# Performance work log

Measured on AMD Instinct MI355X. Metric: run time of the kernel, lower is better.

## Reference

```python
import jax, jax.numpy as jnp
import numpy as np

EPS = 1e-12  # torch F.normalize eps


def setup_inputs() -> dict:
    key = jax.random.key(0)
    k1, k2, k3 = jax.random.split(key, 3)
    B, way, shot, D, H, W = 64, 5, 1, 640, 5, 5
    nq = 75
    base = jax.random.normal(k1, (B, way, shot, D, H, W), dtype=jnp.float32)
    query = jax.random.normal(k2, (B, nq, D, H, W), dtype=jnp.float32)
    r = jax.random.normal(k3, (2,), dtype=jnp.float32) * 0.1
    return {"base": base, "query": query, "r": r, "neighbor_k": 5}


def reference(base, query, r, neighbor_k):
    B, way, shot, D, H, W = base.shape
    nq = query.shape[1]
    hw = H * W

    # ---- global-cosine branch: spatial-mean descriptors ----
    base_mean = base.reshape(B, way * shot, D, hw).mean(axis=-1)   # [B, way*shot, D]
    query_mean = query.reshape(B, nq, D, hw).mean(axis=-1)         # [B, nq, D]
    bm = base_mean / jnp.maximum(jnp.linalg.norm(base_mean, axis=-1, keepdims=True), EPS)
    qm = query_mean / jnp.maximum(jnp.linalg.norm(query_mean, axis=-1, keepdims=True), EPS)
    logits = jnp.einsum('bqd,bkd->bqk', qm, bm)                    # [B, nq, way*shot]

    # ---- DN4 image-to-class branch (vectorized over the original triple loop) ----
    # query local descriptors: [B, nq, hw, D], L2-normalized over channels
    q = query.reshape(B, nq, D, hw).transpose(0, 1, 3, 2)
    q = q / jnp.linalg.norm(q, axis=-1, keepdims=True)
    # support local descriptors: base_mix [B, way, shot*D, hw], column-normalized
    s = base.reshape(B, way, shot * D, hw)
    s = s / jnp.linalg.norm(s, axis=2, keepdims=True)
    # cosine sims between every query patch and every support patch of each class
    # (requires shot*D == D, i.e. shot == 1, as in the original code)
    sim = jnp.einsum('bqpd,bkdl->bqkpl', q, s)                     # [B, nq, way, hw, hw]
    topk_vals, _ = jax.lax.top_k(sim, neighbor_k)                  # [B, nq, way, hw, k]
    logits_dn4 = topk_vals.sum(axis=(-1, -2)) / neighbor_k         # [B, nq, way]

    return r[0] * logits + r[1] * logits_dn4
```

## Files before the change

kernel.cpp:

```cpp
#include <hip/hip_runtime.h>
#include <hip/hip_bf16.h>
#include <math.h>

#define NB    64
#define WAY   5
#define DCH   640
#define HW    25
#define NQ    75
#define NBK   5
#define EPSN  1e-12f

#define QPB   4
#define BPB   ((NQ + QPB - 1) / QPB)
#define NWK   (NB * BPB)
#define NDG   (DCH / 8)
#define SCOLS 128
#define CD    64
#define NCHK  (DCH / CD)
#define CFL   (CD * HW)

typedef __attribute__((ext_vector_type(8)))  short  bf16x8;
typedef __attribute__((ext_vector_type(8)))  ushort u16x8;
typedef __attribute__((ext_vector_type(16))) float  f32x16;
typedef __attribute__((ext_vector_type(4)))  float  f32x4;

#define AS1 __attribute__((address_space(1)))
#define AS3 __attribute__((address_space(3)))

__device__ inline ushort f2bf(float f) {
    uint u = __float_as_uint(f);
    return (ushort)((u + 0x7FFFu + ((u >> 16) & 1u)) >> 16);
}

__global__ __launch_bounds__(256) void k_prep(const float* __restrict__ base,
                                              float* __restrict__ invs,
                                              float* __restrict__ invsm,
                                              ushort* __restrict__ sT)
{
    const int bk = blockIdx.x;
    const int b  = bk / WAY;
    const int k  = bk - b * WAY;
    const float* src = base + (size_t)bk * (DCH * HW);
    __shared__ float lds[DCH * HW];
    __shared__ float red[256];
    const int tid = threadIdx.x;

    const f32x4* s4 = (const f32x4*)src;
    f32x4* l4 = (f32x4*)lds;
    for (int i = tid; i < (DCH * HW) / 4; i += 256)
        l4[i] = __builtin_nontemporal_load(s4 + i);
    __syncthreads();

    if (tid < HW) {
        float ss = 0.f;
        for (int d = 0; d < DCH; ++d) { float v = lds[d * HW + tid]; ss = fmaf(v, v, ss); }
        invs[bk * HW + tid] = rsqrtf(ss);
    }

    float ssq = 0.f;
    for (int d = tid; d < DCH; d += 256) {
        float s = 0.f;
        #pragma unroll
        for (int pp = 0; pp < HW; ++pp) s += lds[d * HW + pp];
        float m = s * (1.0f / HW);
        ssq = fmaf(m, m, ssq);
    }
    red[tid] = ssq;
    __syncthreads();
    for (int s = 128; s > 0; s >>= 1) {
        if (tid < s) red[tid] += red[tid + s];
        __syncthreads();
    }
    if (tid == 0) invsm[bk] = 1.0f / fmaxf(sqrtf(red[0]), EPSN);

    ushort* dstb = sT + (size_t)b * (NDG * SCOLS * 8);
    for (int t = tid; t < NDG * HW; t += 256) {
        const int dg = t / HW, l = t - dg * HW;
        u16x8 v;
        #pragma unroll
        for (int e = 0; e < 8; ++e) v[e] = f2bf(lds[(dg * 8 + e) * HW + l]);
        *(u16x8*)&dstb[((size_t)dg * SCOLS + k * HW + l) * 8] = v;
    }
    if (k == 0) {
        const u16x8 z = (u16x8)(ushort)0;
        for (int t = tid; t < NDG * 3; t += 256) {
            const int dg = t / 3, sc = 125 + (t - dg * 3);
            *(u16x8*)&dstb[((size_t)dg * SCOLS + sc) * 8] = z;
        }
    }
}

__global__ __launch_bounds__(256, 2) void k_fused(const float* __restrict__ query,
                                                  const ushort* __restrict__ sT,
                                                  const float* __restrict__ invs,
                                                  const float* __restrict__ invsm,
                                                  const float* __restrict__ r,
                                                  float* __restrict__ out)
{
    __shared__ __align__(16) float lds_q[QPB][2][CFL];
    __shared__ float invs_l[SCOLS];
    __shared__ float invsm_l[WAY];

    const int tid  = threadIdx.x;
    const int wid  = tid >> 6;
    const int lane = tid & 63;
    const int p    = lane & 31;
    const int hi   = lane >> 5;

    const int wk = (blockIdx.x & 7) * (int)(gridDim.x >> 3) + (blockIdx.x >> 3);
    const int b  = wk / BPB;
    const int qb = wk - b * BPB;
    const int q  = qb * QPB + wid;
    const bool qok = q < NQ;

    if (tid < WAY * HW) invs_l[tid] = invs[b * WAY * HW + tid];
    if (tid >= WAY * HW && tid < SCOLS) invs_l[tid] = 0.f;
    if (tid < WAY)      invsm_l[tid] = invsm[b * WAY + tid];
    __syncthreads();
    if (!qok) return;

    f32x16 acc0 = {}, acc1 = {}, acc2 = {}, acc3 = {}, accg = {};

    const int pc = (p < HW) ? p : (HW - 1);
    const float* qrow = query + (size_t)(b * NQ + q) * (DCH * HW);
    const ushort* sTb = sT + (size_t)b * (NDG * SCOLS * 8);

#define ISSUE(c)                                                               \
    {                                                                          \
        const float* src_ = qrow + (c) * CFL;                                  \
        float* dst_ = &lds_q[wid][(c) & 1][0];                                 \
        _Pragma("unroll")                                                      \
        for (int i = 0; i < 6; ++i)                                            \
            __builtin_amdgcn_global_load_lds(                                  \
                (const AS1 uint*)(src_ + i * 256 + lane * 4),                  \
                (AS3 uint*)(dst_ + i * 256), 16, 0, 0);                        \
        if (lane < 16)                                                         \
            __builtin_amdgcn_global_load_lds(                                  \
                (const AS1 uint*)(src_ + 1536 + lane * 4),                     \
                (AS3 uint*)(dst_ + 1536), 16, 0, 0);                           \
    }

    ISSUE(0)

    for (int c = 0; c < NCHK; ++c) {
        bf16x8 af[16];
        #pragma unroll
        for (int ks = 0; ks < CD / 16; ++ks) {
            const int dg = c * 8 + ks * 2 + hi;
            const bf16x8* arow = (const bf16x8*)(sTb + (size_t)dg * SCOLS * 8);
            af[ks * 4 + 0] = arow[p];
            af[ks * 4 + 1] = arow[32 + p];
            af[ks * 4 + 2] = arow[64 + p];
            af[ks * 4 + 3] = arow[96 + p];
        }

        if (c + 1 < NCHK) {
            asm volatile("s_waitcnt lgkmcnt(0)" ::: "memory");
            ISSUE(c + 1)
            asm volatile("s_waitcnt vmcnt(7)" ::: "memory");
        } else {
            asm volatile("s_waitcnt vmcnt(0)" ::: "memory");
        }
        __builtin_amdgcn_sched_barrier(0);

        const float* qb_lds = &lds_q[wid][c & 1][hi * 8 * HW + pc];
        #pragma unroll
        for (int ks = 0; ks < CD / 16; ++ks) {
            const float v0 = qb_lds[(ks * 16 + 0) * HW];
            const float v1 = qb_lds[(ks * 16 + 1) * HW];
            const float v2 = qb_lds[(ks * 16 + 2) * HW];
            const float v3 = qb_lds[(ks * 16 + 3) * HW];
            const float v4 = qb_lds[(ks * 16 + 4) * HW];
            const float v5 = qb_lds[(ks * 16 + 5) * HW];
            const float v6 = qb_lds[(ks * 16 + 6) * HW];
            const float v7 = qb_lds[(ks * 16 + 7) * HW];
            union { uint u[4]; bf16x8 v; } bqu;
            asm("v_cvt_pk_bf16_f32 %0, %1, %2" : "=v"(bqu.u[0]) : "v"(v0), "v"(v1));
            asm("v_cvt_pk_bf16_f32 %0, %1, %2" : "=v"(bqu.u[1]) : "v"(v2), "v"(v3));
            asm("v_cvt_pk_bf16_f32 %0, %1, %2" : "=v"(bqu.u[2]) : "v"(v4), "v"(v5));
            asm("v_cvt_pk_bf16_f32 %0, %1, %2" : "=v"(bqu.u[3]) : "v"(v6), "v"(v7));
            const bf16x8 bq = bqu.v;
            acc0 = __builtin_amdgcn_mfma_f32_32x32x16_bf16(af[ks * 4 + 0], bq, acc0, 0, 0, 0);
            acc1 = __builtin_amdgcn_mfma_f32_32x32x16_bf16(af[ks * 4 + 1], bq, acc1, 0, 0, 0);
            acc2 = __builtin_amdgcn_mfma_f32_32x32x16_bf16(af[ks * 4 + 2], bq, acc2, 0, 0, 0);
            acc3 = __builtin_amdgcn_mfma_f32_32x32x16_bf16(af[ks * 4 + 3], bq, acc3, 0, 0, 0);
            accg = __builtin_amdgcn_mfma_f32_32x32x16_bf16(bq, bq, accg, 0, 0, 0);
        }
    }
#undef ISSUE

    const bool pok = p < HW;

    float diag = 0.f, qq = 0.f;
    #pragma unroll
    for (int rr = 0; rr < 16; ++rr) {
        const int rowb = (rr & 3) + 8 * (rr >> 2);
        const int row  = rowb + 4 * hi;
        diag = (row == p) ? accg[rr] : diag;
        if (row < HW && pok) qq += accg[rr];
    }
    diag += __shfl_xor(diag, 32);
    const float invq = rsqrtf(diag);

    float gs[WAY] = {0.f, 0.f, 0.f, 0.f, 0.f};
#define TILE_SUM(ACC, T)                                            \
    _Pragma("unroll")                                               \
    for (int rr = 0; rr < 16; ++rr) {                               \
        const int s0 = (T) * 32 + (rr & 3) + 8 * (rr >> 2);         \
        const float v0 = (hi || !pok) ? 0.f : ACC[rr];              \
        const float v1 = (hi && pok) ? ACC[rr] : 0.f;               \
        if (s0 < 125)     gs[s0 / 25]       += v0;                  \
        if (s0 + 4 < 125) gs[(s0 + 4) / 25] += v1;                  \
    }
    TILE_SUM(acc0, 0) TILE_SUM(acc1, 1) TILE_SUM(acc2, 2) TILE_SUM(acc3, 3)
#undef TILE_SUM

    #pragma unroll
    for (int o = 1; o < 64; o <<= 1) {
        qq += __shfl_xor(qq, o);
        #pragma unroll
        for (int g = 0; g < WAY; ++g) gs[g] += __shfl_xor(gs[g], o);
    }

#define SCALE(ACC, T)                                               \
    _Pragma("unroll")                                               \
    for (int rr = 0; rr < 16; ++rr) {                               \
        const int s0 = (T) * 32 + (rr & 3) + 8 * (rr >> 2);         \
        ACC[rr] *= invs_l[s0 + 4 * hi];                             \
    }
    SCALE(acc0, 0) SCALE(acc1, 1) SCALE(acc2, 2) SCALE(acc3, 3)
#undef SCALE

    float tots[WAY];
    #pragma unroll
    for (int g = 0; g < WAY; ++g) {
        float t0 = -3.402823466e38f, t1 = t0, t2 = t0, t3 = t0, t4 = t0;
        #pragma unroll
        for (int j = 0; j < HW; ++j) {
            const int scol = g * HW + j;
            const int t = scol >> 5, row = scol & 31;
            const int hreq = (row >> 2) & 1;
            const int rr = (row & 3) | ((row >> 3) << 2);
            const float av = (t == 0) ? acc0[rr] : (t == 1) ? acc1[rr]
                           : (t == 2) ? acc2[rr] : acc3[rr];
            float mine = (hi == hreq) ? av : 0.f;
            mine += __shfl_xor(mine, 32);
            float x = mine, a;
            a = fmaxf(t0, x); x = fminf(t0, x); t0 = a;
            a = fmaxf(t1, x); x = fminf(t1, x); t1 = a;
            a = fmaxf(t2, x); x = fminf(t2, x); t2 = a;
            a = fmaxf(t3, x); x = fminf(t3, x); t3 = a;
            a = fmaxf(t4, x); x = fminf(t4, x); t4 = a;
        }
        tots[g] = pok ? (t0 + t1 + t2 + t3 + t4) * invq : 0.f;
    }
    #pragma unroll
    for (int o = 1; o < 64; o <<= 1) {
        #pragma unroll
        for (int g = 0; g < WAY; ++g) tots[g] += __shfl_xor(tots[g], o);
    }

    const float r0 = r[0], r1 = r[1];
    const float invqm = 1.0f / fmaxf(sqrtf(qq) * (1.0f / HW), EPSN);
    float res[WAY];
    #pragma unroll
    for (int g = 0; g < WAY; ++g)
        res[g] = r0 * gs[g] * (1.0f / 625.0f) * invqm * invsm_l[g]
               + r1 * tots[g] * 0.5f * (1.0f / NBK);

    float ov = res[0];
    ov = (lane == 1) ? res[1] : ov;
    ov = (lane == 2) ? res[2] : ov;
    ov = (lane == 3) ? res[3] : ov;
    ov = (lane == 4) ? res[4] : ov;
    if (lane < WAY) out[(size_t)(b * NQ + q) * WAY + lane] = ov;
}

extern "C" void kernel_launch(void* const* d_in, const int* in_sizes, int n_in,
                              void* d_out, int out_size, void* d_ws, size_t ws_size,
                              hipStream_t stream)
{
    const float* base  = (const float*)d_in[0];
    const float* query = (const float*)d_in[1];
    const float* r     = (const float*)d_in[2];
    float* out = (float*)d_out;

    float* invs   = (float*)d_ws;
    float* invsm  = invs + NB * WAY * HW;
    ushort* sT    = (ushort*)((float*)d_ws + 16384);

    k_prep<<<NB * WAY, 256, 0, stream>>>(base, invs, invsm, sT);
    k_fused<<<NWK, 256, 0, stream>>>(query, sT, invs, invsm, r, out);
}
```

Before: 112.0 us.

## Double-buffer support fragments in registers and halve query chunk size

Halves the channel chunk staged in LDS and prefetches the next chunk's bf16 support fragments into a second register bank while the current chunk's MFMAs run. The loop is manually unrolled by two to alternate banks, the vmcnt wait is adjusted to cover both queued loads, and setprio raises wave priority during the MFMA block. This aims to hide global-load latency of the support fragments, which was previously exposed at the start of each chunk. It adds more loop iterations and waits, and it can raise register pressure.

```diff
diff --git a/kernel.cpp b/kernel.cpp
--- a/kernel.cpp
+++ b/kernel.cpp
@@ -15,7 +15,7 @@
 #define NWK   (NB * BPB)
 #define NDG   (DCH / 8)
 #define SCOLS 128
-#define CD    64
+#define CD    32
 #define NCHK  (DCH / CD)
 #define CFL   (CD * HW)
 
@@ -130,64 +130,85 @@
         const float* src_ = qrow + (c) * CFL;                                  \
         float* dst_ = &lds_q[wid][(c) & 1][0];                                 \
         _Pragma("unroll")                                                      \
-        for (int i = 0; i < 6; ++i)                                            \
+        for (int i = 0; i < 3; ++i)                                            \
             __builtin_amdgcn_global_load_lds(                                  \
                 (const AS1 uint*)(src_ + i * 256 + lane * 4),                  \
                 (AS3 uint*)(dst_ + i * 256), 16, 0, 0);                        \
-        if (lane < 16)                                                         \
+        if (lane < 8)                                                          \
             __builtin_amdgcn_global_load_lds(                                  \
-                (const AS1 uint*)(src_ + 1536 + lane * 4),                     \
-                (AS3 uint*)(dst_ + 1536), 16, 0, 0);                           \
-    }
-
+                (const AS1 uint*)(src_ + 768 + lane * 4),                      \
+                (AS3 uint*)(dst_ + 768), 16, 0, 0);                            \
+    }
+
+#define LOAD_AF(BANK, c)                                                       \
+    {                                                                          \
+        _Pragma("unroll")                                                      \
+        for (int ks = 0; ks < 2; ++ks) {                                       \
+            const int dg = (c) * 4 + ks * 2 + hi;                              \
+            const bf16x8* arow = (const bf16x8*)(sTb + (size_t)dg * SCOLS * 8);\
+            BANK[ks * 4 + 0] = arow[p];                                        \
+            BANK[ks * 4 + 1] = arow[32 + p];                                   \
+            BANK[ks * 4 + 2] = arow[64 + p];                                   \
+            BANK[ks * 4 + 3] = arow[96 + p];                                   \
+        }                                                                      \
+    }
+
+#define COMPUTE(c, BANK)                                                       \
+    {                                                                          \
+        __builtin_amdgcn_s_setprio(1);                                         \
+        const float* qb_lds = &lds_q[wid][(c) & 1][hi * 8 * HW + pc];          \
+        _Pragma("unroll")                                                      \
+        for (int ks = 0; ks < 2; ++ks) {                                       \
+            const float v0 = qb_lds[(ks * 16 + 0) * HW];                       \
+            const float v1 = qb_lds[(ks * 16 + 1) * HW];                       \
+            const float v2 = qb_lds[(ks * 16 + 2) * HW];                       \
+            const float v3 = qb_lds[(ks * 16 + 3) * HW];                       \
+            const float v4 = qb_lds[(ks * 16 + 4) * HW];                       \
+            const float v5 = qb_lds[(ks * 16 + 5) * HW];                       \
+            const float v6 = qb_lds[(ks * 16 + 6) * HW];                       \
+            const float v7 = qb_lds[(ks * 16 + 7) * HW];                       \
+            union { uint u[4]; bf16x8 v; } bqu;                                \
+            asm("v_cvt_pk_bf16_f32 %0, %1, %2" : "=v"(bqu.u[0]) : "v"(v0), "v"(v1)); \
+            asm("v_cvt_pk_bf16_f32 %0, %1, %2" : "=v"(bqu.u[1]) : "v"(v2), "v"(v3)); \
+            asm("v_cvt_pk_bf16_f32 %0, %1, %2" : "=v"(bqu.u[2]) : "v"(v4), "v"(v5)); \
+            asm("v_cvt_pk_bf16_f32 %0, %1, %2" : "=v"(bqu.u[3]) : "v"(v6), "v"(v7)); \
+            const bf16x8 bq = bqu.v;                                           \
+            acc0 = __builtin_amdgcn_mfma_f32_32x32x16_bf16(BANK[ks * 4 + 0], bq, acc0, 0, 0, 0); \
+            acc1 = __builtin_amdgcn_mfma_f32_32x32x16_bf16(BANK[ks * 4 + 1], bq, acc1, 0, 0, 0); \
+            acc2 = __builtin_amdgcn_mfma_f32_32x32x16_bf16(BANK[ks * 4 + 2], bq, acc2, 0, 0, 0); \
+            acc3 = __builtin_amdgcn_mfma_f32_32x32x16_bf16(BANK[ks * 4 + 3], bq, acc3, 0, 0, 0); \
+            accg = __builtin_amdgcn_mfma_f32_32x32x16_bf16(bq, bq, accg, 0, 0, 0); \
+        }                                                                      \
+        __builtin_amdgcn_s_setprio(0);                                         \
+    }
+
+#define STEP(c, CUR, NXT)                                                      \
+    {                                                                          \
+        if ((c) + 1 < NCHK) {                                                  \
+            asm volatile("s_waitcnt lgkmcnt(0)" ::: "memory");                 \
+            ISSUE((c) + 1)                                                     \
+            LOAD_AF(NXT, (c) + 1)                                              \
+            asm volatile("s_waitcnt vmcnt(12)" ::: "memory");                  \
+        } else {                                                               \
+            asm volatile("s_waitcnt vmcnt(0)" ::: "memory");                   \
+        }                                                                      \
+        __builtin_amdgcn_sched_barrier(0);                                     \
+        COMPUTE(c, CUR)                                                        \
+    }
+
+    bf16x8 afA[8], afB[8];
     ISSUE(0)
-
-    for (int c = 0; c < NCHK; ++c) {
-        bf16x8 af[16];
-        #pragma unroll
-        for (int ks = 0; ks < CD / 16; ++ks) {
-            const int dg = c * 8 + ks * 2 + hi;
-            const bf16x8* arow = (const bf16x8*)(sTb + (size_t)dg * SCOLS * 8);
-            af[ks * 4 + 0] = arow[p];
-            af[ks * 4 + 1] = arow[32 + p];
-            af[ks * 4 + 2] = arow[64 + p];
-            af[ks * 4 + 3] = arow[96 + p];
-        }
-
-        if (c + 1 < NCHK) {
-            asm volatile("s_waitcnt lgkmcnt(0)" ::: "memory");
-            ISSUE(c + 1)
-            asm volatile("s_waitcnt vmcnt(7)" ::: "memory");
-        } else {
-            asm volatile("s_waitcnt vmcnt(0)" ::: "memory");
-        }
-        __builtin_amdgcn_sched_barrier(0);
-
-        const float* qb_lds = &lds_q[wid][c & 1][hi * 8 * HW + pc];
-        #pragma unroll
-        for (int ks = 0; ks < CD / 16; ++ks) {
-            const float v0 = qb_lds[(ks * 16 + 0) * HW];
-            const float v1 = qb_lds[(ks * 16 + 1) * HW];
-            const float v2 = qb_lds[(ks * 16 + 2) * HW];
-            const float v3 = qb_lds[(ks * 16 + 3) * HW];
-            const float v4 = qb_lds[(ks * 16 + 4) * HW];
-            const float v5 = qb_lds[(ks * 16 + 5) * HW];
-            const float v6 = qb_lds[(ks * 16 + 6) * HW];
-            const float v7 = qb_lds[(ks * 16 + 7) * HW];
-            union { uint u[4]; bf16x8 v; } bqu;
-            asm("v_cvt_pk_bf16_f32 %0, %1, %2" : "=v"(bqu.u[0]) : "v"(v0), "v"(v1));
-            asm("v_cvt_pk_bf16_f32 %0, %1, %2" : "=v"(bqu.u[1]) : "v"(v2), "v"(v3));
-            asm("v_cvt_pk_bf16_f32 %0, %1, %2" : "=v"(bqu.u[2]) : "v"(v4), "v"(v5));
-            asm("v_cvt_pk_bf16_f32 %0, %1, %2" : "=v"(bqu.u[3]) : "v"(v6), "v"(v7));
-            const bf16x8 bq = bqu.v;
-            acc0 = __builtin_amdgcn_mfma_f32_32x32x16_bf16(af[ks * 4 + 0], bq, acc0, 0, 0, 0);
-            acc1 = __builtin_amdgcn_mfma_f32_32x32x16_bf16(af[ks * 4 + 1], bq, acc1, 0, 0, 0);
-            acc2 = __builtin_amdgcn_mfma_f32_32x32x16_bf16(af[ks * 4 + 2], bq, acc2, 0, 0, 0);
-            acc3 = __builtin_amdgcn_mfma_f32_32x32x16_bf16(af[ks * 4 + 3], bq, acc3, 0, 0, 0);
-            accg = __builtin_amdgcn_mfma_f32_32x32x16_bf16(bq, bq, accg, 0, 0, 0);
-        }
+    LOAD_AF(afA, 0)
+
+    #pragma unroll 1
+    for (int c = 0; c < NCHK; c += 2) {
+        STEP(c,     afA, afB)
+        STEP(c + 1, afB, afA)
     }
 #undef ISSUE
+#undef LOAD_AF
+#undef COMPUTE
+#undef STEP
 
     const bool pok = p < HW;
 
```

After: 108.0 us (median of 2 runs). -3.6%, faster.
